# Kernel tuning notes

Hardware: AMD Instinct MI355X
Metric: run time of the kernel (lower is better)

Reference implementation:

```python
import jax, jax.numpy as jnp
import numpy as np

BANDWIDTH = 0.1
NUM_ITERS = 5


def setup_inputs() -> dict:
    key = jax.random.key(0)
    # image batch in [0,1], BCHW
    x = jax.random.uniform(key, (2, 3, 96, 96), dtype=jnp.float32)
    return {"x": x}


def reference(x):
    # Mean-shift filtering: each pixel feature y is iteratively moved to the
    # Gaussian-kernel weighted mean of ALL original pixel features:
    #   y_{t+1} = sum_j exp(-||y_t - x_j||^2 / (2 bw^2)) x_j / sum_j exp(...)
    B, C, H, W = x.shape
    N = H * W
    pts = x.reshape(B, C, N).transpose(0, 2, 1)  # [B, N, C] original points
    inv2bw2 = jnp.float32(1.0 / (2.0 * BANDWIDTH * BANDWIDTH))
    x_sq = jnp.sum(pts * pts, axis=-1)  # [B, N]

    def step(y, _):
        # squared pairwise distances via ||y||^2 + ||x||^2 - 2 y.x  -> [B, N, N]
        y_sq = jnp.sum(y * y, axis=-1)  # [B, N]
        d2 = y_sq[:, :, None] + x_sq[:, None, :] - 2.0 * jnp.einsum(
            'bnc,bmc->bnm', y, pts)
        w = jnp.exp(-jnp.maximum(d2, 0.0) * inv2bw2)  # Gaussian kernel weights
        num = jnp.einsum('bnm,bmc->bnc', w, pts)  # weighted sum of points
        den = jnp.sum(w, axis=-1, keepdims=True)  # normalizer (>= 1, self-weight)
        return num / den, None

    y, _ = jax.lax.scan(step, pts, None, length=NUM_ITERS)
    return y.transpose(0, 2, 1).reshape(B, C, H, W)
```

## Files before the change

kernel.cpp:

```cpp
#include <hip/hip_runtime.h>
#include <math.h>


typedef float v2f __attribute__((ext_vector_type(2)));

#define NPTS   9216
#define NB     2
#define TOT    (NB * NPTS)
#define MSPLIT 32
#define SLICE  (NPTS / MSPLIT)
#define WSLICE (SLICE / 4)
#define NPB    256
#define NTILES (NPTS / NPB)
#define LOG2E  1.44269504088896340736f

__device__ __forceinline__ v2f splat2(float v) { return (v2f){v, v}; }


__global__ __launch_bounds__(256, 4) void ms_iter(const float* __restrict__ x,
                                                  const float4* __restrict__ accIn,
                                                  float4* __restrict__ accOut,
                                                  float s, int first) {
    __shared__ float4 smem[1024];
    float* const xs = (float*)smem;
    float* const ys = xs + SLICE;
    float* const zs = ys + SLICE;
    float* const ws = zs + SLICE;
    float4* const ypar = smem + SLICE;
    float4* const red  = smem;

    const int tid  = threadIdx.x;
    const int lane = tid & 63;
    const int wv   = tid >> 6;
    const int k    = blockIdx.x % MSPLIT;
    const int tile = blockIdx.x / MSPLIT;
    const int b    = tile / NTILES;
    const int nt   = tile - b * NTILES;
    const int nbase = nt * NPB;
    const float* xb = x + b * 3 * NPTS;
    const int mbeg = k * SLICE;

    for (int i = tid; i < SLICE; i += 256) {
        int g = mbeg + i;
        float px = xb[g] * s;
        float py = xb[NPTS + g] * s;
        float pz = xb[2 * NPTS + g] * s;
        xs[i] = 2.f * px;
        ys[i] = 2.f * py;
        zs[i] = 2.f * pz;
        ws[i] = -fmaf(px, px, fmaf(py, py, pz * pz));
    }
    {
        float y0, y1, y2;
        if (first) {
            int n = nbase + tid;
            y0 = xb[n] * s; y1 = xb[NPTS + n] * s; y2 = xb[2 * NPTS + n] * s;
        } else {
            float4 a = accIn[b * NPTS + nbase + tid];
            float inv = 1.0f / a.w;
            y0 = a.x * inv; y1 = a.y * inv; y2 = a.z * inv;
        }
        ypar[tid] = make_float4(y0, y1, y2,
                                -fmaf(y0, y0, fmaf(y1, y1, y2 * y2)));
    }
    __syncthreads();

    v2f Yx[4], Yy[4], Yz[4], Yw[4], Ax[4], Ay[4], Az[4], Aw[4];
#pragma unroll
    for (int j = 0; j < 4; ++j) {
        float4 yp = ypar[lane + 64 * j];
        Yx[j] = splat2(yp.x); Yy[j] = splat2(yp.y);
        Yz[j] = splat2(yp.z); Yw[j] = splat2(yp.w);
        Ax[j] = splat2(0.f); Ay[j] = splat2(0.f);
        Az[j] = splat2(0.f); Aw[j] = splat2(0.f);
    }

    const float* xsw = xs + wv * WSLICE;
    const float* ysw = ys + wv * WSLICE;
    const float* zsw = zs + wv * WSLICE;
    const float* wsw = ws + wv * WSLICE;

    float4 PX = *(const float4*)(xsw);
    float4 PY = *(const float4*)(ysw);
    float4 PZ = *(const float4*)(zsw);
    float4 PW = *(const float4*)(wsw);
    for (int i = 0; i < WSLICE; i += 4) {
        float4 NX = *(const float4*)(xsw + i + 4);
        float4 NY = *(const float4*)(ysw + i + 4);
        float4 NZ = *(const float4*)(zsw + i + 4);
        float4 NW = *(const float4*)(wsw + i + 4);
        v2f px0 = (v2f){PX.x, PX.y}, px1 = (v2f){PX.z, PX.w};
        v2f py0 = (v2f){PY.x, PY.y}, py1 = (v2f){PY.z, PY.w};
        v2f pz0 = (v2f){PZ.x, PZ.y}, pz1 = (v2f){PZ.z, PZ.w};
        v2f pw0 = (v2f){PW.x, PW.y}, pw1 = (v2f){PW.z, PW.w};
#pragma unroll
        for (int j = 0; j < 4; ++j) {
            v2f t0 = pw0 + Yw[j];
            t0 = __builtin_elementwise_fma(pz0, Yz[j], t0);
            t0 = __builtin_elementwise_fma(py0, Yy[j], t0);
            t0 = __builtin_elementwise_fma(px0, Yx[j], t0);
            v2f t1 = pw1 + Yw[j];
            t1 = __builtin_elementwise_fma(pz1, Yz[j], t1);
            t1 = __builtin_elementwise_fma(py1, Yy[j], t1);
            t1 = __builtin_elementwise_fma(px1, Yx[j], t1);
            v2f w0, w1;
            w0.x = __builtin_amdgcn_exp2f(t0.x);
            w0.y = __builtin_amdgcn_exp2f(t0.y);
            w1.x = __builtin_amdgcn_exp2f(t1.x);
            w1.y = __builtin_amdgcn_exp2f(t1.y);
            Ax[j] = __builtin_elementwise_fma(w0, px0, Ax[j]);
            Ay[j] = __builtin_elementwise_fma(w0, py0, Ay[j]);
            Az[j] = __builtin_elementwise_fma(w0, pz0, Az[j]);
            Aw[j] += w0;
            Ax[j] = __builtin_elementwise_fma(w1, px1, Ax[j]);
            Ay[j] = __builtin_elementwise_fma(w1, py1, Ay[j]);
            Az[j] = __builtin_elementwise_fma(w1, pz1, Az[j]);
            Aw[j] += w1;
        }
        PX = NX; PY = NY; PZ = NZ; PW = NW;
    }

    __syncthreads();
#pragma unroll
    for (int j = 0; j < 4; ++j) {
        red[wv * NPB + lane + 64 * j] =
            make_float4(Ax[j].x + Ax[j].y, Ay[j].x + Ay[j].y,
                        Az[j].x + Az[j].y, Aw[j].x + Aw[j].y);
    }
    __syncthreads();
    {
        float4 r0 = red[tid];
        float4 r1 = red[NPB + tid];
        float4 r2 = red[2 * NPB + tid];
        float4 r3 = red[3 * NPB + tid];
        float ox = 0.5f * ((r0.x + r1.x) + (r2.x + r3.x));
        float oy = 0.5f * ((r0.y + r1.y) + (r2.y + r3.y));
        float oz = 0.5f * ((r0.z + r1.z) + (r2.z + r3.z));
        float od = (r0.w + r1.w) + (r2.w + r3.w);
        float* dst = (float*)&accOut[b * NPTS + nbase + tid];
        atomicAdd(dst + 0, ox);
        atomicAdd(dst + 1, oy);
        atomicAdd(dst + 2, oz);
        atomicAdd(dst + 3, od);
    }
}

__global__ __launch_bounds__(256) void ms_pack(const float4* __restrict__ acc4,
                                               float* __restrict__ out,
                                               float invs) {
    int gid = blockIdx.x * 256 + threadIdx.x;
    int b = gid / NPTS;
    int n = gid - b * NPTS;
    float4 a = acc4[gid];
    float f = invs / a.w;
    float* ob = out + b * 3 * NPTS;
    ob[n]            = a.x * f;
    ob[NPTS + n]     = a.y * f;
    ob[2 * NPTS + n] = a.z * f;
}

extern "C" void kernel_launch(void* const* d_in, const int* in_sizes, int n_in,
                              void* d_out, int out_size, void* d_ws, size_t ws_size,
                              hipStream_t stream) {
    const float* x = (const float*)d_in[0];
    float* out = (float*)d_out;
    float s = sqrtf(50.0f * LOG2E);

    float4* acc = (float4*)d_ws;

    hipMemsetAsync(acc, 0, (size_t)5 * TOT * sizeof(float4), stream);

    for (int it = 0; it < 5; ++it) {
        const float4* accIn = (it == 0) ? nullptr : acc + (size_t)(it - 1) * TOT;
        ms_iter<<<NB * NTILES * MSPLIT, 256, 0, stream>>>(
            x, accIn, acc + (size_t)it * TOT, s, it == 0 ? 1 : 0);
    }
    ms_pack<<<TOT / 256, 256, 0, stream>>>(acc + (size_t)4 * TOT, out, 1.0f / s);
}
```

Measured before the change: 236.3 us.

## Fuse all mean-shift iterations into one persistent kernel with per-group barriers

Replaces the five per-iteration launches and the final pack kernel with a single kernel that loops over iterations. Blocks that share a 256-point output tile sync through an atomic counter barrier, so each group moves on as soon as its own slice sums are complete, without a device-wide wait. MSPLIT drops from 32 to 16 so the grid (1152 blocks at up to 5 per CU) can be co-resident, which the spin barrier needs. The cost is fewer, longer blocks per tile, spin-wait overhead, and a deadlock risk if not all blocks in a group are resident at once.

```diff
diff --git a/kernel.cpp b/kernel.cpp
--- a/kernel.cpp
+++ b/kernel.cpp
@@ -7,156 +7,171 @@
 #define NPTS   9216
 #define NB     2
 #define TOT    (NB * NPTS)
-#define MSPLIT 32
+#define MSPLIT 16
 #define SLICE  (NPTS / MSPLIT)
 #define WSLICE (SLICE / 4)
 #define NPB    256
 #define NTILES (NPTS / NPB)
+#define NGRP   (NB * NTILES)
+#define GRIDSZ (NGRP * MSPLIT)
 #define LOG2E  1.44269504088896340736f
 
 __device__ __forceinline__ v2f splat2(float v) { return (v2f){v, v}; }
 
 
-__global__ __launch_bounds__(256, 4) void ms_iter(const float* __restrict__ x,
-                                                  const float4* __restrict__ accIn,
-                                                  float4* __restrict__ accOut,
-                                                  float s, int first) {
-    __shared__ float4 smem[1024];
-    float* const xs = (float*)smem;
+__device__ __forceinline__ void group_barrier(int* ctr, int target) {
+    __syncthreads();
+    if (threadIdx.x == 0) {
+        __threadfence();
+        atomicAdd(ctr, 1);
+        while (atomicAdd(ctr, 0) < target)
+            __builtin_amdgcn_s_sleep(2);
+        __threadfence();
+    }
+    __syncthreads();
+}
+
+__global__ __launch_bounds__(256, 5) void ms_all(const float* __restrict__ x,
+                                                 float4* __restrict__ acc,
+                                                 int* __restrict__ bars,
+                                                 float* __restrict__ out,
+                                                 float s) {
+    __shared__ float smem[4096];
+    float* const xs = smem;
     float* const ys = xs + SLICE;
     float* const zs = ys + SLICE;
     float* const ws = zs + SLICE;
-    float4* const ypar = smem + SLICE;
-    float4* const red  = smem;
+    float4* const ypar = (float4*)(smem + 4 * SLICE);
+    float4* const red  = (float4*)smem;
 
     const int tid  = threadIdx.x;
     const int lane = tid & 63;
     const int wv   = tid >> 6;
     const int k    = blockIdx.x % MSPLIT;
-    const int tile = blockIdx.x / MSPLIT;
-    const int b    = tile / NTILES;
-    const int nt   = tile - b * NTILES;
+    const int grp  = blockIdx.x / MSPLIT;
+    const int b    = grp / NTILES;
+    const int nt   = grp - b * NTILES;
     const int nbase = nt * NPB;
     const float* xb = x + b * 3 * NPTS;
     const int mbeg = k * SLICE;
+    int* const ctr = bars + grp * 16;
 
-    for (int i = tid; i < SLICE; i += 256) {
-        int g = mbeg + i;
-        float px = xb[g] * s;
-        float py = xb[NPTS + g] * s;
-        float pz = xb[2 * NPTS + g] * s;
-        xs[i] = 2.f * px;
-        ys[i] = 2.f * py;
-        zs[i] = 2.f * pz;
-        ws[i] = -fmaf(px, px, fmaf(py, py, pz * pz));
-    }
-    {
-        float y0, y1, y2;
-        if (first) {
-            int n = nbase + tid;
-            y0 = xb[n] * s; y1 = xb[NPTS + n] * s; y2 = xb[2 * NPTS + n] * s;
-        } else {
-            float4 a = accIn[b * NPTS + nbase + tid];
-            float inv = 1.0f / a.w;
-            y0 = a.x * inv; y1 = a.y * inv; y2 = a.z * inv;
+    for (int it = 0; it < 5; ++it) {
+        for (int i = tid; i < SLICE; i += 256) {
+            int g = mbeg + i;
+            float px = xb[g] * s;
+            float py = xb[NPTS + g] * s;
+            float pz = xb[2 * NPTS + g] * s;
+            xs[i] = 2.f * px;
+            ys[i] = 2.f * py;
+            zs[i] = 2.f * pz;
+            ws[i] = -fmaf(px, px, fmaf(py, py, pz * pz));
         }
-        ypar[tid] = make_float4(y0, y1, y2,
-                                -fmaf(y0, y0, fmaf(y1, y1, y2 * y2)));
-    }
-    __syncthreads();
+        {
+            float y0, y1, y2;
+            if (it == 0) {
+                int n = nbase + tid;
+                y0 = xb[n] * s; y1 = xb[NPTS + n] * s; y2 = xb[2 * NPTS + n] * s;
+            } else {
+                float4 a = acc[(size_t)(it - 1) * TOT + b * NPTS + nbase + tid];
+                float inv = 1.0f / a.w;
+                y0 = a.x * inv; y1 = a.y * inv; y2 = a.z * inv;
+            }
+            ypar[tid] = make_float4(y0, y1, y2,
+                                    -fmaf(y0, y0, fmaf(y1, y1, y2 * y2)));
+        }
+        __syncthreads();
 
-    v2f Yx[4], Yy[4], Yz[4], Yw[4], Ax[4], Ay[4], Az[4], Aw[4];
+        v2f Yx[4], Yy[4], Yz[4], Yw[4], Ax[4], Ay[4], Az[4], Aw[4];
 #pragma unroll
-    for (int j = 0; j < 4; ++j) {
-        float4 yp = ypar[lane + 64 * j];
-        Yx[j] = splat2(yp.x); Yy[j] = splat2(yp.y);
-        Yz[j] = splat2(yp.z); Yw[j] = splat2(yp.w);
-        Ax[j] = splat2(0.f); Ay[j] = splat2(0.f);
-        Az[j] = splat2(0.f); Aw[j] = splat2(0.f);
+        for (int j = 0; j < 4; ++j) {
+            float4 yp = ypar[lane + 64 * j];
+            Yx[j] = splat2(yp.x); Yy[j] = splat2(yp.y);
+            Yz[j] = splat2(yp.z); Yw[j] = splat2(yp.w);
+            Ax[j] = splat2(0.f); Ay[j] = splat2(0.f);
+            Az[j] = splat2(0.f); Aw[j] = splat2(0.f);
+        }
+
+        const float* xsw = xs + wv * WSLICE;
+        const float* ysw = ys + wv * WSLICE;
+        const float* zsw = zs + wv * WSLICE;
+        const float* wsw = ws + wv * WSLICE;
+
+        float4 PX = *(const float4*)(xsw);
+        float4 PY = *(const float4*)(ysw);
+        float4 PZ = *(const float4*)(zsw);
+        float4 PW = *(const float4*)(wsw);
+        for (int i = 0; i < WSLICE; i += 4) {
+            float4 NX = *(const float4*)(xsw + i + 4);
+            float4 NY = *(const float4*)(ysw + i + 4);
+            float4 NZ = *(const float4*)(zsw + i + 4);
+            float4 NW = *(const float4*)(wsw + i + 4);
+            v2f px0 = (v2f){PX.x, PX.y}, px1 = (v2f){PX.z, PX.w};
+            v2f py0 = (v2f){PY.x, PY.y}, py1 = (v2f){PY.z, PY.w};
+            v2f pz0 = (v2f){PZ.x, PZ.y}, pz1 = (v2f){PZ.z, PZ.w};
+            v2f pw0 = (v2f){PW.x, PW.y}, pw1 = (v2f){PW.z, PW.w};
+#pragma unroll
+            for (int j = 0; j < 4; ++j) {
+                v2f t0 = pw0 + Yw[j];
+                t0 = __builtin_elementwise_fma(pz0, Yz[j], t0);
+                t0 = __builtin_elementwise_fma(py0, Yy[j], t0);
+                t0 = __builtin_elementwise_fma(px0, Yx[j], t0);
+                v2f t1 = pw1 + Yw[j];
+                t1 = __builtin_elementwise_fma(pz1, Yz[j], t1);
+                t1 = __builtin_elementwise_fma(py1, Yy[j], t1);
+                t1 = __builtin_elementwise_fma(px1, Yx[j], t1);
+                v2f w0, w1;
+                w0.x = __builtin_amdgcn_exp2f(t0.x);
+                w0.y = __builtin_amdgcn_exp2f(t0.y);
+                w1.x = __builtin_amdgcn_exp2f(t1.x);
+                w1.y = __builtin_amdgcn_exp2f(t1.y);
+                Ax[j] = __builtin_elementwise_fma(w0, px0, Ax[j]);
+                Ay[j] = __builtin_elementwise_fma(w0, py0, Ay[j]);
+                Az[j] = __builtin_elementwise_fma(w0, pz0, Az[j]);
+                Aw[j] += w0;
+                Ax[j] = __builtin_elementwise_fma(w1, px1, Ax[j]);
+                Ay[j] = __builtin_elementwise_fma(w1, py1, Ay[j]);
+                Az[j] = __builtin_elementwise_fma(w1, pz1, Az[j]);
+                Aw[j] += w1;
+            }
+            PX = NX; PY = NY; PZ = NZ; PW = NW;
+        }
+
+        __syncthreads();
+#pragma unroll
+        for (int j = 0; j < 4; ++j) {
+            red[wv * NPB + lane + 64 * j] =
+                make_float4(Ax[j].x + Ax[j].y, Ay[j].x + Ay[j].y,
+                            Az[j].x + Az[j].y, Aw[j].x + Aw[j].y);
+        }
+        __syncthreads();
+        {
+            float4 r0 = red[tid];
+            float4 r1 = red[NPB + tid];
+            float4 r2 = red[2 * NPB + tid];
+            float4 r3 = red[3 * NPB + tid];
+            float ox = 0.5f * ((r0.x + r1.x) + (r2.x + r3.x));
+            float oy = 0.5f * ((r0.y + r1.y) + (r2.y + r3.y));
+            float oz = 0.5f * ((r0.z + r1.z) + (r2.z + r3.z));
+            float od = (r0.w + r1.w) + (r2.w + r3.w);
+            float* dst = (float*)&acc[(size_t)it * TOT + b * NPTS + nbase + tid];
+            atomicAdd(dst + 0, ox);
+            atomicAdd(dst + 1, oy);
+            atomicAdd(dst + 2, oz);
+            atomicAdd(dst + 3, od);
+        }
+        group_barrier(ctr, (it + 1) * MSPLIT);
     }
 
-    const float* xsw = xs + wv * WSLICE;
-    const float* ysw = ys + wv * WSLICE;
-    const float* zsw = zs + wv * WSLICE;
-    const float* wsw = ws + wv * WSLICE;
-
-    float4 PX = *(const float4*)(xsw);
-    float4 PY = *(const float4*)(ysw);
-    float4 PZ = *(const float4*)(zsw);
-    float4 PW = *(const float4*)(wsw);
-    for (int i = 0; i < WSLICE; i += 4) {
-        float4 NX = *(const float4*)(xsw + i + 4);
-        float4 NY = *(const float4*)(ysw + i + 4);
-        float4 NZ = *(const float4*)(zsw + i + 4);
-        float4 NW = *(const float4*)(wsw + i + 4);
-        v2f px0 = (v2f){PX.x, PX.y}, px1 = (v2f){PX.z, PX.w};
-        v2f py0 = (v2f){PY.x, PY.y}, py1 = (v2f){PY.z, PY.w};
-        v2f pz0 = (v2f){PZ.x, PZ.y}, pz1 = (v2f){PZ.z, PZ.w};
-        v2f pw0 = (v2f){PW.x, PW.y}, pw1 = (v2f){PW.z, PW.w};
-#pragma unroll
-        for (int j = 0; j < 4; ++j) {
-            v2f t0 = pw0 + Yw[j];
-            t0 = __builtin_elementwise_fma(pz0, Yz[j], t0);
-            t0 = __builtin_elementwise_fma(py0, Yy[j], t0);
-            t0 = __builtin_elementwise_fma(px0, Yx[j], t0);
-            v2f t1 = pw1 + Yw[j];
-            t1 = __builtin_elementwise_fma(pz1, Yz[j], t1);
-            t1 = __builtin_elementwise_fma(py1, Yy[j], t1);
-            t1 = __builtin_elementwise_fma(px1, Yx[j], t1);
-            v2f w0, w1;
-            w0.x = __builtin_amdgcn_exp2f(t0.x);
-            w0.y = __builtin_amdgcn_exp2f(t0.y);
-            w1.x = __builtin_amdgcn_exp2f(t1.x);
-            w1.y = __builtin_amdgcn_exp2f(t1.y);
-            Ax[j] = __builtin_elementwise_fma(w0, px0, Ax[j]);
-            Ay[j] = __builtin_elementwise_fma(w0, py0, Ay[j]);
-            Az[j] = __builtin_elementwise_fma(w0, pz0, Az[j]);
-            Aw[j] += w0;
-            Ax[j] = __builtin_elementwise_fma(w1, px1, Ax[j]);
-            Ay[j] = __builtin_elementwise_fma(w1, py1, Ay[j]);
-            Az[j] = __builtin_elementwise_fma(w1, pz1, Az[j]);
-            Aw[j] += w1;
-        }
-        PX = NX; PY = NY; PZ = NZ; PW = NW;
+    if (k == 0) {
+        int n = nbase + tid;
+        float4 a = acc[(size_t)4 * TOT + b * NPTS + n];
+        float f = 1.0f / (s * a.w);
+        float* ob = out + b * 3 * NPTS;
+        ob[n]            = a.x * f;
+        ob[NPTS + n]     = a.y * f;
+        ob[2 * NPTS + n] = a.z * f;
     }
-
-    __syncthreads();
-#pragma unroll
-    for (int j = 0; j < 4; ++j) {
-        red[wv * NPB + lane + 64 * j] =
-            make_float4(Ax[j].x + Ax[j].y, Ay[j].x + Ay[j].y,
-                        Az[j].x + Az[j].y, Aw[j].x + Aw[j].y);
-    }
-    __syncthreads();
-    {
-        float4 r0 = red[tid];
-        float4 r1 = red[NPB + tid];
-        float4 r2 = red[2 * NPB + tid];
-        float4 r3 = red[3 * NPB + tid];
-        float ox = 0.5f * ((r0.x + r1.x) + (r2.x + r3.x));
-        float oy = 0.5f * ((r0.y + r1.y) + (r2.y + r3.y));
-        float oz = 0.5f * ((r0.z + r1.z) + (r2.z + r3.z));
-        float od = (r0.w + r1.w) + (r2.w + r3.w);
-        float* dst = (float*)&accOut[b * NPTS + nbase + tid];
-        atomicAdd(dst + 0, ox);
-        atomicAdd(dst + 1, oy);
-        atomicAdd(dst + 2, oz);
-        atomicAdd(dst + 3, od);
-    }
-}
-
-__global__ __launch_bounds__(256) void ms_pack(const float4* __restrict__ acc4,
-                                               float* __restrict__ out,
-                                               float invs) {
-    int gid = blockIdx.x * 256 + threadIdx.x;
-    int b = gid / NPTS;
-    int n = gid - b * NPTS;
-    float4 a = acc4[gid];
-    float f = invs / a.w;
-    float* ob = out + b * 3 * NPTS;
-    ob[n]            = a.x * f;
-    ob[NPTS + n]     = a.y * f;
-    ob[2 * NPTS + n] = a.z * f;
 }
 
 extern "C" void kernel_launch(void* const* d_in, const int* in_sizes, int n_in,
@@ -167,13 +182,11 @@
     float s = sqrtf(50.0f * LOG2E);
 
     float4* acc = (float4*)d_ws;
+    int* bars = (int*)(acc + (size_t)5 * TOT);
 
-    hipMemsetAsync(acc, 0, (size_t)5 * TOT * sizeof(float4), stream);
+    hipMemsetAsync(acc, 0,
+                   (size_t)5 * TOT * sizeof(float4) + NGRP * 16 * sizeof(int),
+                   stream);
 
-    for (int it = 0; it < 5; ++it) {
-        const float4* accIn = (it == 0) ? nullptr : acc + (size_t)(it - 1) * TOT;
-        ms_iter<<<NB * NTILES * MSPLIT, 256, 0, stream>>>(
-            x, accIn, acc + (size_t)it * TOT, s, it == 0 ? 1 : 0);
-    }
-    ms_pack<<<TOT / 256, 256, 0, stream>>>(acc + (size_t)4 * TOT, out, 1.0f / s);
+    ms_all<<<GRIDSZ, 256, 0, stream>>>(x, acc, bars, out, s);
 }
```

Measured after the change: 318.3 us. 1.35x slower.
